# Kernel optimization log

Hardware: AMD Instinct MI355X
Metric: run time of the kernel (lower is better)

The kernel has to match this reference:

```python
import jax, jax.numpy as jnp
import numpy as np

HEADS = 16
SEG = 512


def setup_inputs() -> dict:
    key = jax.random.key(0)
    kx, k1, k2, k3, k4, k5 = jax.random.split(key, 6)
    B, L, D = 4, 8192, 1024
    scale = 1.0 / np.sqrt(D).astype(np.float32)
    return {
        "x": jax.random.normal(kx, (B, L, D), jnp.float32),
        "mask": jnp.ones((B, 1, 1, L), jnp.int32),
        "wq": jax.random.normal(k1, (D, D), jnp.float32) * scale,
        "wk": jax.random.normal(k2, (D, D), jnp.float32) * scale,
        "wv": jax.random.normal(k3, (D, D), jnp.float32) * scale,
        "wo_w": jax.random.normal(k4, (D, D), jnp.float32) * scale,
        "wo_b": jnp.zeros((D,), jnp.float32),
        "betas": jax.random.normal(k5, (1, HEADS, 1, D // HEADS), jnp.float32),
    }


def reference(x, mask, wq, wk, wv, wo_w, wo_b, betas):
    B, L, D = x.shape
    H = HEADS
    dk = D // H
    S = SEG
    nseg = L // S
    inv_sqrt_dk = jnp.asarray(1.0 / np.sqrt(dk), x.dtype)

    def proj(w):  # torch Linear: x @ W^T -> (B,H,L,dk)
        return (x @ w.T).reshape(B, L, H, dk).transpose(0, 2, 1, 3)

    q, k, v = proj(wq), proj(wk), proj(wv)

    # chunk into segments: (nseg, B, H, S, dk)
    def seg(t):
        return t.reshape(B, H, nseg, S, dk).transpose(2, 0, 1, 3, 4)

    qs, ksg, vs = seg(q), seg(k), seg(v)
    ms = mask.reshape(B, 1, 1, nseg, S).transpose(3, 0, 1, 2, 4)  # (nseg,B,1,1,S)

    gate = jax.nn.sigmoid(betas)  # (1,H,1,dk)

    def body(carry, inp):
        mem, z = carry  # mem: (B,H,dk,dk), z: (B,H,dk)
        qg, kg, vg, mg = inp
        # segment-local SDPA
        scores = jnp.einsum("bhsd,bhtd->bhst", qg, kg) * inv_sqrt_dk
        scores = jnp.where(mg == 0, jnp.asarray(-1e9, scores.dtype), scores)
        A_dot = jnp.einsum("bhst,bhtd->bhsd", jax.nn.softmax(scores, axis=-1), vg)
        # memory read with old state
        aq = jax.nn.elu(qg) + 1.0
        denom = jnp.einsum("bhsd,bhd->bhs", aq, z)[..., None] + 1e-9
        A_mem = jnp.einsum("bhsd,bhde->bhse", aq, mem) / denom
        # linear memory update
        ak = jax.nn.elu(kg) + 1.0
        mem = mem + jnp.einsum("bhsd,bhse->bhde", ak, vg)
        z = z + ak.sum(axis=2)
        att = gate * A_mem + (1.0 - gate) * A_dot
        return (mem, z), att

    mem0 = jnp.zeros((B, H, dk, dk), x.dtype)
    z0 = jnp.zeros((B, H, dk), x.dtype)
    _, ys = jax.lax.scan(body, (mem0, z0), (qs, ksg, vs, ms))
    # (nseg,B,H,S,dk) -> (B, L, D)
    out = ys.transpose(1, 0, 3, 2, 4).reshape(B, L, D)
    return out @ wo_w.T + wo_b
```

## Files before the change

### kernel.cpp

```cpp
#include <hip/hip_runtime.h>

typedef float fv2 __attribute__((ext_vector_type(2)));
typedef float fv4 __attribute__((ext_vector_type(4)));
typedef _Float16 hfv8 __attribute__((ext_vector_type(8)));
typedef unsigned short u16v4 __attribute__((ext_vector_type(4)));
typedef unsigned short u16v8 __attribute__((ext_vector_type(8)));

#define B_DIM 4
#define L_DIM 8192
#define D_DIM 1024
#define H_NUM 16
#define NSEG 16
#define SEG_S 512
#define M_TOK (B_DIM * L_DIM)

__device__ __forceinline__ unsigned short f2h(float f) {
  return __builtin_bit_cast(unsigned short, (_Float16)f);
}
__device__ __forceinline__ float h2f(unsigned short u) {
  return (float)__builtin_bit_cast(_Float16, u);
}

__global__ __launch_bounds__(256) void conv_w16(
    const float* __restrict__ in, unsigned short* __restrict__ outp, int n4) {
  int i = blockIdx.x * 256 + threadIdx.x;
  const int stride = gridDim.x * 256;
  for (; i < n4; i += stride) {
    fv4 v = reinterpret_cast<const fv4*>(in)[i];
    u16v4 p;
#pragma unroll
    for (int j = 0; j < 4; ++j) p[j] = f2h(v[j]);
    reinterpret_cast<u16v4*>(outp)[i] = p;
  }
}

template <int QKV>
__global__ __launch_bounds__(256, 2) void gemm_bt(
    const _Float16* __restrict__ A16, const _Float16* __restrict__ B16,
    float* __restrict__ C, const float* __restrict__ bias,
    unsigned short* __restrict__ Oq, unsigned short* __restrict__ Ok,
    unsigned short* __restrict__ Ov, int M, int NTILES, int K) {
  __shared__ _Float16 sA[3][8192];
  __shared__ _Float16 sB[3][4096];
  const int tid = threadIdx.x;
  const int lane = tid & 63;
  const int wv = tid >> 6;
  const int wr = wv >> 1, wc = wv & 1;
  const int g = lane >> 4, ln16 = lane & 15;

  const int hw = blockIdx.x;
  const int xcd = hw & 7;
  const int rem = hw >> 3;
  const int ntile = rem % NTILES;
  const int yhi = rem / NTILES;
  const int mtile = yhi * 8 + xcd;
  const int mBase = mtile * 256;
  const int nBase = ntile * 128;

  fv4 acc[8][4] = {};

  const int srow = lane >> 2;
  const int cgx = ((lane & 3) ^ ((lane >> 3) & 3)) * 8;
  const long aStageBase = (long)(mBase + wv * 64 + srow) * K + cgx;
  const long bStageBase = (long)(nBase + wv * 32 + srow) * K + cgx;
  const int rgx = (g ^ ((ln16 >> 1) & 3)) * 8;
  const int arow0 = wr * 128 + ln16;
  const int brow0 = wc * 64 + ln16;

  auto STAGE = [&](int t, int bi) {
#pragma unroll
    for (int i = 0; i < 4; ++i)
      __builtin_amdgcn_global_load_lds(
          (const __attribute__((address_space(1))) void*)(A16 + aStageBase + (long)i * 16 * K + t * 32),
          (__attribute__((address_space(3))) void*)&sA[bi][wv * 2048 + i * 512], 16, 0, 0);
#pragma unroll
    for (int i = 0; i < 2; ++i)
      __builtin_amdgcn_global_load_lds(
          (const __attribute__((address_space(1))) void*)(B16 + bStageBase + (long)i * 16 * K + t * 32),
          (__attribute__((address_space(3))) void*)&sB[bi][wv * 1024 + i * 512], 16, 0, 0);
  };
  auto COMPUTE = [&](int bi) {
    hfv8 fa[8], fb[4];
#pragma unroll
    for (int i = 0; i < 4; ++i)
      fa[i] = *(const hfv8*)&sA[bi][(arow0 + i * 16) * 32 + rgx];
    fb[0] = *(const hfv8*)&sB[bi][(brow0) * 32 + rgx];
    fb[1] = *(const hfv8*)&sB[bi][(brow0 + 16) * 32 + rgx];
    __builtin_amdgcn_s_setprio(1);
#pragma unroll
    for (int i = 0; i < 4; ++i)
#pragma unroll
      for (int j = 0; j < 2; ++j)
        acc[i][j] = __builtin_amdgcn_mfma_f32_16x16x32_f16(fa[i], fb[j], acc[i][j], 0, 0, 0);
    __builtin_amdgcn_s_setprio(0);
    fb[2] = *(const hfv8*)&sB[bi][(brow0 + 32) * 32 + rgx];
    fb[3] = *(const hfv8*)&sB[bi][(brow0 + 48) * 32 + rgx];
    __builtin_amdgcn_s_setprio(1);
#pragma unroll
    for (int i = 0; i < 4; ++i)
#pragma unroll
      for (int j = 2; j < 4; ++j)
        acc[i][j] = __builtin_amdgcn_mfma_f32_16x16x32_f16(fa[i], fb[j], acc[i][j], 0, 0, 0);
    __builtin_amdgcn_s_setprio(0);
#pragma unroll
    for (int i = 4; i < 8; ++i)
      fa[i] = *(const hfv8*)&sA[bi][(arow0 + i * 16) * 32 + rgx];
    __builtin_amdgcn_s_setprio(1);
#pragma unroll
    for (int i = 4; i < 8; ++i)
#pragma unroll
      for (int j = 0; j < 2; ++j)
        acc[i][j] = __builtin_amdgcn_mfma_f32_16x16x32_f16(fa[i], fb[j], acc[i][j], 0, 0, 0);
#pragma unroll
    for (int i = 4; i < 8; ++i)
#pragma unroll
      for (int j = 2; j < 4; ++j)
        acc[i][j] = __builtin_amdgcn_mfma_f32_16x16x32_f16(fa[i], fb[j], acc[i][j], 0, 0, 0);
    __builtin_amdgcn_s_setprio(0);
  };

  const int NT = K / 32;
  STAGE(0, 0);
  STAGE(1, 1);
  for (int t = 0; t < NT; ++t) {
    if (t < NT - 1)
      asm volatile("s_waitcnt vmcnt(6)" ::: "memory");
    else
      asm volatile("s_waitcnt vmcnt(0)" ::: "memory");
    __builtin_amdgcn_s_barrier();
    if (t + 2 < NT) STAGE(t + 2, (t + 2) % 3);
    COMPUTE(t % 3);
    asm volatile("s_waitcnt lgkmcnt(0)" ::: "memory");
  }

  const int crow0 = mBase + wr * 128 + ((lane >> 4) << 2);
  const int ccol0 = nBase + wc * 64 + (lane & 15);
  if (QKV) {
    const int which = nBase >> 10;
    unsigned short* outs = (which == 0) ? Oq : (which == 1) ? Ok : Ov;
    const int colb = ccol0 & 1023;
#pragma unroll
    for (int j = 0; j < 4; ++j) {
      const int col = colb + j * 16;
#pragma unroll
      for (int i = 0; i < 8; ++i) {
        const long rb = (long)(crow0 + i * 16) * 1024 + col;
#pragma unroll
        for (int r = 0; r < 4; ++r)
          outs[rb + (long)r * 1024] = f2h(acc[i][j][r]);
      }
    }
  } else {
    float bv[4];
#pragma unroll
    for (int j = 0; j < 4; ++j) bv[j] = bias ? bias[ccol0 + j * 16] : 0.f;
#pragma unroll
    for (int j = 0; j < 4; ++j) {
      const int col = ccol0 + j * 16;
#pragma unroll
      for (int i = 0; i < 8; ++i) {
        const long rb = (long)(crow0 + i * 16) * 1024 + col;
#pragma unroll
        for (int r = 0; r < 4; ++r)
          C[rb + (long)r * 1024] = acc[i][j][r] + bv[j];
      }
    }
  }
}

__global__ __launch_bounds__(256) void seg_outer_mfma(
    const unsigned short* __restrict__ K16, const unsigned short* __restrict__ V16,
    float* __restrict__ U, float* __restrict__ Zs) {
  __shared__ _Float16 sAh[64 * 64], sAl[64 * 64];
  __shared__ _Float16 sVh[64 * 64];
  __shared__ float sZf[64];
  const int bid = blockIdx.x;
  const int b = bid >> 8, seg = (bid >> 4) & 15, h = bid & 15;
  const int tid = threadIdx.x;
  const int lane = tid & 63, w = tid >> 6;
  const int g = lane >> 4, ln16 = lane & 15;
  const long base = ((long)b * L_DIM + (long)seg * SEG_S) * D_DIM + h * 64;

  if (tid < 64) sZf[tid] = 0.f;
  fv4 acc[4] = {};
  float zacc = 0.f;
  const int strow = tid & 63;
  const int sg0 = (tid >> 6) * 16;
  const int wsw = (strow & 7) << 3;
  const int rsw = (ln16 & 7) << 3;

  for (int c = 0; c < 8; ++c) {
    __syncthreads();
#pragma unroll
    for (int jj = 0; jj < 2; ++jj) {
      u16v8 ah, al, vh;
#pragma unroll
      for (int i = 0; i < 8; ++i) {
        const long gidx = base + (long)(c * 64 + sg0 + jj * 8 + i) * D_DIM + strow;
        const float kv = h2f(K16[gidx]);
        const float a = kv > 0.f ? kv + 1.f : __expf(kv);
        zacc += a;
        const unsigned short hb = f2h(a);
        ah[i] = hb;
        al[i] = f2h(a - h2f(hb));
        vh[i] = V16[gidx];
      }
      const int col = (sg0 + jj * 8) ^ wsw;
      *(u16v8*)&sAh[strow * 64 + col] = ah;
      *(u16v8*)&sAl[strow * 64 + col] = al;
      *(u16v8*)&sVh[strow * 64 + col] = vh;
    }
    __syncthreads();
#pragma unroll
    for (int kf = 0; kf < 2; ++kf) {
      const int so = (kf * 32 + g * 8) ^ rsw;
      hfv8 aH = *(const hfv8*)&sAh[(w * 16 + ln16) * 64 + so];
      hfv8 aL = *(const hfv8*)&sAl[(w * 16 + ln16) * 64 + so];
      __builtin_amdgcn_s_setprio(1);
#pragma unroll
      for (int et = 0; et < 4; ++et) {
        hfv8 bH = *(const hfv8*)&sVh[(et * 16 + ln16) * 64 + so];
        acc[et] = __builtin_amdgcn_mfma_f32_16x16x32_f16(aH, bH, acc[et], 0, 0, 0);
        acc[et] = __builtin_amdgcn_mfma_f32_16x16x32_f16(aL, bH, acc[et], 0, 0, 0);
      }
      __builtin_amdgcn_s_setprio(0);
    }
  }
  atomicAdd(&sZf[strow], zacc);
  __syncthreads();

  const long ub = (long)bid * 4096;
#pragma unroll
  for (int et = 0; et < 4; ++et)
#pragma unroll
    for (int r = 0; r < 4; ++r)
      U[ub + (long)(w * 16 + g * 4 + r) * 64 + et * 16 + ln16] = acc[et][r];
  if (tid < 64) Zs[(long)bid * 64 + tid] = sZf[tid];
}

__global__ __launch_bounds__(256) void seg_prefix(
    const float* __restrict__ U, const float* __restrict__ Zs,
    float* __restrict__ Mem, float* __restrict__ Zp) {
  const int bh = blockIdx.x;
  const int b = bh >> 4, h = bh & 15;
  const int jc = blockIdx.y;
  const int tid = threadIdx.x;
  for (int j = jc * 512 + tid; j < jc * 512 + 512; j += 256) {
    float run = 0.f;
#pragma unroll
    for (int t = 0; t < NSEG; ++t) {
      const long idx = ((long)(b * 256 + t * 16 + h)) * 4096 + j;
      Mem[idx] = run;
      run += U[idx];
    }
  }
  if (jc == 0 && tid < 64) {
    float run = 0.f;
#pragma unroll
    for (int t = 0; t < NSEG; ++t) {
      const long idx = ((long)(b * 256 + t * 16 + h)) * 64 + tid;
      Zp[idx] = run;
      run += Zs[idx];
    }
  }
}

__global__ __launch_bounds__(512, 4) void attn_seg_mfma(
    const unsigned short* __restrict__ Q16, const unsigned short* __restrict__ K16,
    const unsigned short* __restrict__ V16, const int* __restrict__ mask,
    const float* __restrict__ Mem, const float* __restrict__ Zp,
    const float* __restrict__ betas, unsigned short* __restrict__ Op16) {
  __shared__ _Float16 sKh[64 * 72];
  __shared__ _Float16 sVTh[64 * 64];
  __shared__ _Float16 sP[8][16 * 72];
  __shared__ float sMadd[64], sZ[64], sGate[64];

  const int bx = (blockIdx.x & 7) * 512 + (blockIdx.x >> 3);
  const int qblk = bx & 3, h = (bx >> 2) & 15, seg = (bx >> 6) & 15, b = bx >> 10;
  const int shb = b * 256 + seg * 16 + h;
  const int tid = threadIdx.x;
  const int lane = tid & 63, w = tid >> 6;
  const int g = lane >> 4, ln16 = lane & 15;
  const int rsw = (ln16 & 7) << 3;

  const int qglob = b * L_DIM + seg * SEG_S + qblk * 128 + w * 16 + ln16;
  const long qbase = (long)qglob * D_DIM + h * 64;
  hfv8 qh[2];
#pragma unroll
  for (int dt = 0; dt < 2; ++dt)
    qh[dt] = *(const hfv8*)&Q16[qbase + dt * 32 + g * 8];

  fv4 O[4] = {};
  float m_run = -1e30f, l_run = 0.f;
  const long kvbase0 = ((long)b * L_DIM + (long)seg * SEG_S) * D_DIM + h * 64;

  for (int c = 0; c < 8; ++c) {
    __syncthreads();
    {
      const int row = tid >> 3, d0 = (tid & 7) * 8;
      const long ga = kvbase0 + (long)(c * 64 + row) * D_DIM + d0;
      *(u16v8*)&sKh[row * 72 + d0] = *(const u16v8*)&K16[ga];
    }
    {
      const int e = tid & 63, kg = (tid >> 6) * 8;
      u16v8 hv;
#pragma unroll
      for (int j = 0; j < 8; ++j)
        hv[j] = V16[kvbase0 + (long)(c * 64 + kg + j) * D_DIM + e];
      *(u16v8*)&sVTh[e * 64 + (kg ^ ((e & 7) << 3))] = hv;
    }
    if (tid < 64)
      sMadd[tid] = (mask[b * L_DIM + seg * SEG_S + c * 64 + tid] == 0) ? -1e9f : 0.f;
    __syncthreads();

    fv4 madd[4];
#pragma unroll
    for (int kt = 0; kt < 4; ++kt) madd[kt] = *(const fv4*)&sMadd[kt * 16 + g * 4];

    fv4 sc[4];
#pragma unroll
    for (int kt = 0; kt < 4; ++kt) {
      const int ro = (kt * 16 + ln16) * 72 + g * 8;
      hfv8 kh0 = *(const hfv8*)&sKh[ro], kh1 = *(const hfv8*)&sKh[ro + 32];
      fv4 s = {};
      __builtin_amdgcn_s_setprio(1);
      s = __builtin_amdgcn_mfma_f32_16x16x32_f16(kh0, qh[0], s, 0, 0, 0);
      s = __builtin_amdgcn_mfma_f32_16x16x32_f16(kh1, qh[1], s, 0, 0, 0);
      __builtin_amdgcn_s_setprio(0);
      sc[kt] = s;
    }
    float pmax = -3.0e38f;
#pragma unroll
    for (int kt = 0; kt < 4; ++kt)
#pragma unroll
      for (int r = 0; r < 4; ++r) {
        const float v = __builtin_fmaf(sc[kt][r], 0.125f, madd[kt][r]);
        sc[kt][r] = v;
        pmax = fmaxf(pmax, v);
      }
    pmax = fmaxf(pmax, __shfl_xor(pmax, 16));
    pmax = fmaxf(pmax, __shfl_xor(pmax, 32));
    if (pmax > m_run + 8.f) {
      const float resc = __expf(m_run - pmax);
      l_run *= resc;
#pragma unroll
      for (int et = 0; et < 4; ++et)
#pragma unroll
        for (int r = 0; r < 4; ++r) O[et][r] *= resc;
      m_run = pmax;
    }
    float psum = 0.f;
#pragma unroll
    for (int kt = 0; kt < 4; ++kt) {
      u16v4 pv;
#pragma unroll
      for (int r = 0; r < 4; ++r) {
        const unsigned short hb = f2h(__expf(sc[kt][r] - m_run));
        pv[r] = hb;
        psum += h2f(hb);
      }
      *(u16v4*)&sP[w][ln16 * 72 + kt * 16 + g * 4] = pv;
    }
    psum += __shfl_xor(psum, 16);
    psum += __shfl_xor(psum, 32);
    l_run += psum;

    hfv8 pf0 = *(const hfv8*)&sP[w][ln16 * 72 + g * 8];
    hfv8 pf1 = *(const hfv8*)&sP[w][ln16 * 72 + 32 + g * 8];
    __builtin_amdgcn_s_setprio(1);
#pragma unroll
    for (int et = 0; et < 4; ++et) {
      const int rb = (et * 16 + ln16) * 64;
      hfv8 vh0 = *(const hfv8*)&sVTh[rb + ((g * 8) ^ rsw)];
      hfv8 vh1 = *(const hfv8*)&sVTh[rb + ((g * 8 + 32) ^ rsw)];
      fv4 o = O[et];
      o = __builtin_amdgcn_mfma_f32_16x16x32_f16(vh0, pf0, o, 0, 0, 0);
      o = __builtin_amdgcn_mfma_f32_16x16x32_f16(vh1, pf1, o, 0, 0, 0);
      O[et] = o;
    }
    __builtin_amdgcn_s_setprio(0);
  }

  __syncthreads();
  {
    const int e2 = (tid & 31) * 2, d4 = (tid >> 5) * 4;
    const float* Memp = Mem + (long)shb * 4096;
    fv2 ld[4];
#pragma unroll
    for (int i = 0; i < 4; ++i) ld[i] = *(const fv2*)&Memp[(d4 + i) * 64 + e2];
#pragma unroll
    for (int je = 0; je < 2; ++je) {
      u16v4 hv;
#pragma unroll
      for (int i = 0; i < 4; ++i) hv[i] = f2h(ld[i][je]);
      *(u16v4*)&sKh[(e2 + je) * 72 + d4] = hv;
    }
  }
  if (tid < 64) {
    sZ[tid] = Zp[(long)shb * 64 + tid];
    sGate[tid] = 1.f / (1.f + __expf(-betas[h * 64 + tid]));
  }
  __syncthreads();

  float dpart = 0.f;
#pragma unroll
  for (int dt = 0; dt < 2; ++dt) {
    u16v8 ah;
#pragma unroll
    for (int j = 0; j < 8; ++j) {
      const float x = (float)qh[dt][j];
      const float a = x > 0.f ? x + 1.f : __expf(x);
      dpart += a * sZ[dt * 32 + g * 8 + j];
      ah[j] = f2h(a);
    }
    qh[dt] = __builtin_bit_cast(hfv8, ah);
  }
  dpart += __shfl_xor(dpart, 16);
  dpart += __shfl_xor(dpart, 32);
  const float invden = 1.f / (dpart + 1e-9f);
  const float invl = 1.f / l_run;

  const long obase = (long)qglob * D_DIM + h * 64;
#pragma unroll
  for (int et = 0; et < 4; ++et) {
    const int ro = (et * 16 + ln16) * 72 + g * 8;
    hfv8 mh0 = *(const hfv8*)&sKh[ro], mh1 = *(const hfv8*)&sKh[ro + 32];
    fv4 o = {};
    o = __builtin_amdgcn_mfma_f32_16x16x32_f16(mh0, qh[0], o, 0, 0, 0);
    o = __builtin_amdgcn_mfma_f32_16x16x32_f16(mh1, qh[1], o, 0, 0, 0);
    const fv4 gt = *(const fv4*)&sGate[et * 16 + g * 4];
    u16v4 st;
#pragma unroll
    for (int r = 0; r < 4; ++r) {
      const float att = gt[r] * o[r] * invden + (1.f - gt[r]) * O[et][r] * invl;
      st[r] = f2h(att);
    }
    *(u16v4*)&Op16[obase + et * 16 + g * 4] = st;
  }
}

extern "C" void kernel_launch(void* const* d_in, const int* in_sizes, int n_in,
                              void* d_out, int out_size, void* d_ws, size_t ws_size,
                              hipStream_t stream) {
  (void)in_sizes; (void)n_in; (void)out_size;
  const float* x     = (const float*)d_in[0];
  const int*   mask  = (const int*)d_in[1];
  const float* wq    = (const float*)d_in[2];
  const float* wk    = (const float*)d_in[3];
  const float* wv    = (const float*)d_in[4];
  const float* wo    = (const float*)d_in[5];
  const float* wob   = (const float*)d_in[6];
  const float* betas = (const float*)d_in[7];
  float* out = (float*)d_out;

  const size_t TOK = (size_t)M_TOK * D_DIM;
  char* ws = (char*)d_ws;
  size_t off = 0;
  auto alloc = [&](size_t bytes) {
    char* p = ws + off;
    off += (bytes + 255) & ~(size_t)255;
    return p;
  };
  unsigned short* wqkv16 = (unsigned short*)alloc((size_t)3 * D_DIM * D_DIM * 2);
  unsigned short* wo16   = (unsigned short*)alloc((size_t)D_DIM * D_DIM * 2);
  unsigned short* x16 = (unsigned short*)alloc(TOK * 2);
  unsigned short* q16 = (unsigned short*)alloc(TOK * 2);
  unsigned short* k16 = (unsigned short*)alloc(TOK * 2);
  unsigned short* v16 = (unsigned short*)alloc(TOK * 2);
  float* U   = (float*)alloc((size_t)B_DIM * NSEG * H_NUM * 4096 * 4);
  float* Mem = (float*)alloc((size_t)B_DIM * NSEG * H_NUM * 4096 * 4);
  float* Zs  = (float*)alloc((size_t)B_DIM * NSEG * H_NUM * 64 * 4);
  float* Zp  = (float*)alloc((size_t)B_DIM * NSEG * H_NUM * 64 * 4);
  unsigned short* att16 = x16;

  if (off > ws_size) return;

  conv_w16<<<256, 256, 0, stream>>>(wq, wqkv16, D_DIM * D_DIM / 4);
  conv_w16<<<256, 256, 0, stream>>>(wk, wqkv16 + (size_t)D_DIM * D_DIM, D_DIM * D_DIM / 4);
  conv_w16<<<256, 256, 0, stream>>>(wv, wqkv16 + (size_t)2 * D_DIM * D_DIM, D_DIM * D_DIM / 4);
  conv_w16<<<256, 256, 0, stream>>>(wo, wo16, D_DIM * D_DIM / 4);
  conv_w16<<<2048, 256, 0, stream>>>(x, x16, (int)(TOK / 4));

  const int qkvGrid = 24 * (M_TOK / 256);
  gemm_bt<1><<<qkvGrid, 256, 0, stream>>>(
      (const _Float16*)x16, (const _Float16*)wqkv16, nullptr, nullptr,
      q16, k16, v16, M_TOK, 24, D_DIM);

  seg_outer_mfma<<<B_DIM * NSEG * H_NUM, 256, 0, stream>>>(k16, v16, U, Zs);
  seg_prefix<<<dim3(B_DIM * H_NUM, 8), 256, 0, stream>>>(U, Zs, Mem, Zp);

  attn_seg_mfma<<<B_DIM * NSEG * H_NUM * 4, 512, 0, stream>>>(
      q16, k16, v16, mask, Mem, Zp, betas, att16);

  const int oGrid = 8 * (M_TOK / 256);
  gemm_bt<0><<<oGrid, 256, 0, stream>>>(
      (const _Float16*)att16, (const _Float16*)wo16, out, wob,
      nullptr, nullptr, nullptr, M_TOK, 8, D_DIM);
}
```

Before: 604.5 us.

## Double-buffer GEMM for higher occupancy; process two query tiles per attention block

The GEMM drops from triple to double buffering in shared memory and raises the launch-bounds occupancy target from 2 to 3 blocks per CU. The prefetch of the next tile is now issued before the wait, and a second barrier per iteration is added. The attention kernel now handles 256 queries per block as two 128-query sub-tiles, so each K/V chunk loaded into shared memory is reused twice and the grid is halved. The costs are more barriers and a shallower prefetch depth in the GEMM, and higher register pressure plus fewer blocks in the attention kernel.

```diff
diff --git a/kernel.cpp b/kernel.cpp
--- a/kernel.cpp
+++ b/kernel.cpp
@@ -35,13 +35,13 @@
 }
 
 template <int QKV>
-__global__ __launch_bounds__(256, 2) void gemm_bt(
+__global__ __launch_bounds__(256, 3) void gemm_bt(
     const _Float16* __restrict__ A16, const _Float16* __restrict__ B16,
     float* __restrict__ C, const float* __restrict__ bias,
     unsigned short* __restrict__ Oq, unsigned short* __restrict__ Ok,
     unsigned short* __restrict__ Ov, int M, int NTILES, int K) {
-  __shared__ _Float16 sA[3][8192];
-  __shared__ _Float16 sB[3][4096];
+  __shared__ _Float16 sA[2][8192];
+  __shared__ _Float16 sB[2][4096];
   const int tid = threadIdx.x;
   const int lane = tid & 63;
   const int wv = tid >> 6;
@@ -109,28 +109,24 @@
 #pragma unroll
     for (int i = 4; i < 8; ++i)
 #pragma unroll
-      for (int j = 0; j < 2; ++j)
-        acc[i][j] = __builtin_amdgcn_mfma_f32_16x16x32_f16(fa[i], fb[j], acc[i][j], 0, 0, 0);
-#pragma unroll
-    for (int i = 4; i < 8; ++i)
-#pragma unroll
-      for (int j = 2; j < 4; ++j)
+      for (int j = 0; j < 4; ++j)
         acc[i][j] = __builtin_amdgcn_mfma_f32_16x16x32_f16(fa[i], fb[j], acc[i][j], 0, 0, 0);
     __builtin_amdgcn_s_setprio(0);
   };
 
   const int NT = K / 32;
   STAGE(0, 0);
-  STAGE(1, 1);
   for (int t = 0; t < NT; ++t) {
-    if (t < NT - 1)
+    if (t + 1 < NT) {
+      STAGE(t + 1, (t + 1) & 1);
       asm volatile("s_waitcnt vmcnt(6)" ::: "memory");
-    else
+    } else {
       asm volatile("s_waitcnt vmcnt(0)" ::: "memory");
+    }
     __builtin_amdgcn_s_barrier();
-    if (t + 2 < NT) STAGE(t + 2, (t + 2) % 3);
-    COMPUTE(t % 3);
+    COMPUTE(t & 1);
     asm volatile("s_waitcnt lgkmcnt(0)" ::: "memory");
+    __builtin_amdgcn_s_barrier();
   }
 
   const int crow0 = mBase + wr * 128 + ((lane >> 4) << 2);
@@ -275,23 +271,27 @@
   __shared__ _Float16 sP[8][16 * 72];
   __shared__ float sMadd[64], sZ[64], sGate[64];
 
-  const int bx = (blockIdx.x & 7) * 512 + (blockIdx.x >> 3);
-  const int qblk = bx & 3, h = (bx >> 2) & 15, seg = (bx >> 6) & 15, b = bx >> 10;
+  const int bx = (blockIdx.x & 7) * 256 + (blockIdx.x >> 3);
+  const int qpair = bx & 1, h = (bx >> 1) & 15, seg = (bx >> 5) & 15, b = bx >> 9;
   const int shb = b * 256 + seg * 16 + h;
   const int tid = threadIdx.x;
   const int lane = tid & 63, w = tid >> 6;
   const int g = lane >> 4, ln16 = lane & 15;
   const int rsw = (ln16 & 7) << 3;
 
-  const int qglob = b * L_DIM + seg * SEG_S + qblk * 128 + w * 16 + ln16;
-  const long qbase = (long)qglob * D_DIM + h * 64;
-  hfv8 qh[2];
-#pragma unroll
-  for (int dt = 0; dt < 2; ++dt)
-    qh[dt] = *(const hfv8*)&Q16[qbase + dt * 32 + g * 8];
-
-  fv4 O[4] = {};
-  float m_run = -1e30f, l_run = 0.f;
+  int qglob[2];
+  hfv8 qh[2][2];
+#pragma unroll
+  for (int s = 0; s < 2; ++s) {
+    qglob[s] = b * L_DIM + seg * SEG_S + qpair * 256 + s * 128 + w * 16 + ln16;
+    const long qb = (long)qglob[s] * D_DIM + h * 64;
+#pragma unroll
+    for (int dt = 0; dt < 2; ++dt)
+      qh[s][dt] = *(const hfv8*)&Q16[qb + dt * 32 + g * 8];
+  }
+
+  fv4 O[2][4] = {};
+  float m_run[2] = {-1e30f, -1e30f}, l_run[2] = {0.f, 0.f};
   const long kvbase0 = ((long)b * L_DIM + (long)seg * SEG_S) * D_DIM + h * 64;
 
   for (int c = 0; c < 8; ++c) {
@@ -317,68 +317,71 @@
 #pragma unroll
     for (int kt = 0; kt < 4; ++kt) madd[kt] = *(const fv4*)&sMadd[kt * 16 + g * 4];
 
-    fv4 sc[4];
-#pragma unroll
-    for (int kt = 0; kt < 4; ++kt) {
-      const int ro = (kt * 16 + ln16) * 72 + g * 8;
-      hfv8 kh0 = *(const hfv8*)&sKh[ro], kh1 = *(const hfv8*)&sKh[ro + 32];
-      fv4 s = {};
+#pragma unroll
+    for (int s = 0; s < 2; ++s) {
+      fv4 sc[4];
+#pragma unroll
+      for (int kt = 0; kt < 4; ++kt) {
+        const int ro = (kt * 16 + ln16) * 72 + g * 8;
+        hfv8 kh0 = *(const hfv8*)&sKh[ro], kh1 = *(const hfv8*)&sKh[ro + 32];
+        fv4 sv = {};
+        __builtin_amdgcn_s_setprio(1);
+        sv = __builtin_amdgcn_mfma_f32_16x16x32_f16(kh0, qh[s][0], sv, 0, 0, 0);
+        sv = __builtin_amdgcn_mfma_f32_16x16x32_f16(kh1, qh[s][1], sv, 0, 0, 0);
+        __builtin_amdgcn_s_setprio(0);
+        sc[kt] = sv;
+      }
+      float pmax = -3.0e38f;
+#pragma unroll
+      for (int kt = 0; kt < 4; ++kt)
+#pragma unroll
+        for (int r = 0; r < 4; ++r) {
+          const float v = __builtin_fmaf(sc[kt][r], 0.125f, madd[kt][r]);
+          sc[kt][r] = v;
+          pmax = fmaxf(pmax, v);
+        }
+      pmax = fmaxf(pmax, __shfl_xor(pmax, 16));
+      pmax = fmaxf(pmax, __shfl_xor(pmax, 32));
+      if (pmax > m_run[s] + 8.f) {
+        const float resc = __expf(m_run[s] - pmax);
+        l_run[s] *= resc;
+#pragma unroll
+        for (int et = 0; et < 4; ++et)
+#pragma unroll
+          for (int r = 0; r < 4; ++r) O[s][et][r] *= resc;
+        m_run[s] = pmax;
+      }
+      float psum = 0.f;
+#pragma unroll
+      for (int kt = 0; kt < 4; ++kt) {
+        u16v4 pv;
+#pragma unroll
+        for (int r = 0; r < 4; ++r) {
+          const unsigned short hb = f2h(__expf(sc[kt][r] - m_run[s]));
+          pv[r] = hb;
+          psum += h2f(hb);
+        }
+        *(u16v4*)&sP[w][ln16 * 72 + kt * 16 + g * 4] = pv;
+      }
+      psum += __shfl_xor(psum, 16);
+      psum += __shfl_xor(psum, 32);
+      l_run[s] += psum;
+
+      hfv8 pf0 = *(const hfv8*)&sP[w][ln16 * 72 + g * 8];
+      hfv8 pf1 = *(const hfv8*)&sP[w][ln16 * 72 + 32 + g * 8];
       __builtin_amdgcn_s_setprio(1);
-      s = __builtin_amdgcn_mfma_f32_16x16x32_f16(kh0, qh[0], s, 0, 0, 0);
-      s = __builtin_amdgcn_mfma_f32_16x16x32_f16(kh1, qh[1], s, 0, 0, 0);
+#pragma unroll
+      for (int et = 0; et < 4; ++et) {
+        const int rb = (et * 16 + ln16) * 64;
+        hfv8 vh0 = *(const hfv8*)&sVTh[rb + ((g * 8) ^ rsw)];
+        hfv8 vh1 = *(const hfv8*)&sVTh[rb + ((g * 8 + 32) ^ rsw)];
+        fv4 o = O[s][et];
+        o = __builtin_amdgcn_mfma_f32_16x16x32_f16(vh0, pf0, o, 0, 0, 0);
+        o = __builtin_amdgcn_mfma_f32_16x16x32_f16(vh1, pf1, o, 0, 0, 0);
+        O[s][et] = o;
+      }
       __builtin_amdgcn_s_setprio(0);
-      sc[kt] = s;
-    }
-    float pmax = -3.0e38f;
-#pragma unroll
-    for (int kt = 0; kt < 4; ++kt)
-#pragma unroll
-      for (int r = 0; r < 4; ++r) {
-        const float v = __builtin_fmaf(sc[kt][r], 0.125f, madd[kt][r]);
-        sc[kt][r] = v;
-        pmax = fmaxf(pmax, v);
-      }
-    pmax = fmaxf(pmax, __shfl_xor(pmax, 16));
-    pmax = fmaxf(pmax, __shfl_xor(pmax, 32));
-    if (pmax > m_run + 8.f) {
-      const float resc = __expf(m_run - pmax);
-      l_run *= resc;
-#pragma unroll
-      for (int et = 0; et < 4; ++et)
-#pragma unroll
-        for (int r = 0; r < 4; ++r) O[et][r] *= resc;
-      m_run = pmax;
-    }
-    float psum = 0.f;
-#pragma unroll
-    for (int kt = 0; kt < 4; ++kt) {
-      u16v4 pv;
-#pragma unroll
-      for (int r = 0; r < 4; ++r) {
-        const unsigned short hb = f2h(__expf(sc[kt][r] - m_run));
-        pv[r] = hb;
-        psum += h2f(hb);
-      }
-      *(u16v4*)&sP[w][ln16 * 72 + kt * 16 + g * 4] = pv;
-    }
-    psum += __shfl_xor(psum, 16);
-    psum += __shfl_xor(psum, 32);
-    l_run += psum;
-
-    hfv8 pf0 = *(const hfv8*)&sP[w][ln16 * 72 + g * 8];
-    hfv8 pf1 = *(const hfv8*)&sP[w][ln16 * 72 + 32 + g * 8];
-    __builtin_amdgcn_s_setprio(1);
-#pragma unroll
-    for (int et = 0; et < 4; ++et) {
-      const int rb = (et * 16 + ln16) * 64;
-      hfv8 vh0 = *(const hfv8*)&sVTh[rb + ((g * 8) ^ rsw)];
-      hfv8 vh1 = *(const hfv8*)&sVTh[rb + ((g * 8 + 32) ^ rsw)];
-      fv4 o = O[et];
-      o = __builtin_amdgcn_mfma_f32_16x16x32_f16(vh0, pf0, o, 0, 0, 0);
-      o = __builtin_amdgcn_mfma_f32_16x16x32_f16(vh1, pf1, o, 0, 0, 0);
-      O[et] = o;
-    }
-    __builtin_amdgcn_s_setprio(0);
+    }
   }
 
   __syncthreads();
@@ -402,40 +405,43 @@
   }
   __syncthreads();
 
-  float dpart = 0.f;
-#pragma unroll
-  for (int dt = 0; dt < 2; ++dt) {
-    u16v8 ah;
-#pragma unroll
-    for (int j = 0; j < 8; ++j) {
-      const float x = (float)qh[dt][j];
-      const float a = x > 0.f ? x + 1.f : __expf(x);
-      dpart += a * sZ[dt * 32 + g * 8 + j];
-      ah[j] = f2h(a);
-    }
-    qh[dt] = __builtin_bit_cast(hfv8, ah);
-  }
-  dpart += __shfl_xor(dpart, 16);
-  dpart += __shfl_xor(dpart, 32);
-  const float invden = 1.f / (dpart + 1e-9f);
-  const float invl = 1.f / l_run;
-
-  const long obase = (long)qglob * D_DIM + h * 64;
-#pragma unroll
-  for (int et = 0; et < 4; ++et) {
-    const int ro = (et * 16 + ln16) * 72 + g * 8;
-    hfv8 mh0 = *(const hfv8*)&sKh[ro], mh1 = *(const hfv8*)&sKh[ro + 32];
-    fv4 o = {};
-    o = __builtin_amdgcn_mfma_f32_16x16x32_f16(mh0, qh[0], o, 0, 0, 0);
-    o = __builtin_amdgcn_mfma_f32_16x16x32_f16(mh1, qh[1], o, 0, 0, 0);
-    const fv4 gt = *(const fv4*)&sGate[et * 16 + g * 4];
-    u16v4 st;
-#pragma unroll
-    for (int r = 0; r < 4; ++r) {
-      const float att = gt[r] * o[r] * invden + (1.f - gt[r]) * O[et][r] * invl;
-      st[r] = f2h(att);
-    }
-    *(u16v4*)&Op16[obase + et * 16 + g * 4] = st;
+#pragma unroll
+  for (int s = 0; s < 2; ++s) {
+    float dpart = 0.f;
+#pragma unroll
+    for (int dt = 0; dt < 2; ++dt) {
+      u16v8 ah;
+#pragma unroll
+      for (int j = 0; j < 8; ++j) {
+        const float xv = (float)qh[s][dt][j];
+        const float a = xv > 0.f ? xv + 1.f : __expf(xv);
+        dpart += a * sZ[dt * 32 + g * 8 + j];
+        ah[j] = f2h(a);
+      }
+      qh[s][dt] = __builtin_bit_cast(hfv8, ah);
+    }
+    dpart += __shfl_xor(dpart, 16);
+    dpart += __shfl_xor(dpart, 32);
+    const float invden = 1.f / (dpart + 1e-9f);
+    const float invl = 1.f / l_run[s];
+
+    const long obase = (long)qglob[s] * D_DIM + h * 64;
+#pragma unroll
+    for (int et = 0; et < 4; ++et) {
+      const int ro = (et * 16 + ln16) * 72 + g * 8;
+      hfv8 mh0 = *(const hfv8*)&sKh[ro], mh1 = *(const hfv8*)&sKh[ro + 32];
+      fv4 o = {};
+      o = __builtin_amdgcn_mfma_f32_16x16x32_f16(mh0, qh[s][0], o, 0, 0, 0);
+      o = __builtin_amdgcn_mfma_f32_16x16x32_f16(mh1, qh[s][1], o, 0, 0, 0);
+      const fv4 gt = *(const fv4*)&sGate[et * 16 + g * 4];
+      u16v4 st;
+#pragma unroll
+      for (int r = 0; r < 4; ++r) {
+        const float att = gt[r] * o[r] * invden + (1.f - gt[r]) * O[s][et][r] * invl;
+        st[r] = f2h(att);
+      }
+      *(u16v4*)&Op16[obase + et * 16 + g * 4] = st;
+    }
   }
 }
 
@@ -489,7 +495,7 @@
   seg_outer_mfma<<<B_DIM * NSEG * H_NUM, 256, 0, stream>>>(k16, v16, U, Zs);
   seg_prefix<<<dim3(B_DIM * H_NUM, 8), 256, 0, stream>>>(U, Zs, Mem, Zp);
 
-  attn_seg_mfma<<<B_DIM * NSEG * H_NUM * 4, 512, 0, stream>>>(
+  attn_seg_mfma<<<B_DIM * NSEG * H_NUM * 2, 512, 0, stream>>>(
       q16, k16, v16, mask, Mem, Zp, betas, att16);
 
   const int oGrid = 8 * (M_TOK / 256);
```

Result: slower. 694.5 us (+14.9%).
